# Kernel tuning notes

Measured on AMD Instinct MI355X. Metric: run time of the kernel, lower is better.

## Reference

```python
import jax, jax.numpy as jnp
import numpy as np

SR = 44100        # sample rate (init arg)
WIN = 442         # FFT window length from tensor[i:i+442]
HOP = 4           # loop stride
NBINS = 221       # kept spectrum bins x[:221]
THR = 0.01        # threshold passed to inner fftLayer
REL = 0.0594      # relative pitch-change threshold
BIN_HZ = 100.0    # argmax*100 -> frequency


def _windows_and_mag(tensor):
    n = tensor.shape[0]
    n_win = (n - WIN + HOP - 1) // HOP
    starts = jnp.arange(n_win) * HOP
    windows = tensor[starts[:, None] + jnp.arange(WIN)[None, :]]
    spec = jnp.fft.fft(windows, axis=-1)[:, :NBINS]           # complex64 [n_win, 221]
    spec = jnp.where(jnp.abs(spec) < THR, jnp.zeros_like(spec), spec)  # fftLayer threshold
    mag = jnp.abs(spec.real) + jnp.abs(spec.imag)             # |re| + |im|, as in forward
    return mag, starts


def setup_inputs() -> dict:
    key = jax.random.key(0)
    return {"tensor": jax.random.normal(key, (1_000_000,), dtype=jnp.float32)}


def reference(tensor):
    mag, starts = _windows_and_mag(tensor)
    # per-window dominant frequency: argmax bin * 100 Hz
    tmp = jnp.argmax(mag, axis=-1).astype(jnp.float32) * BIN_HZ    # [n_win]
    i_samp = starts.astype(jnp.float32)                            # sample index of each window

    def step(carry, x):
        maxF, Ftime = carry
        t, i = x
        cond = jnp.abs(maxF - t) > maxF * REL
        emit_f = maxF
        emit_d = (i - Ftime) * 1000.0 / SR
        maxF = jnp.where(cond, t, maxF)
        Ftime = jnp.where(cond, i, Ftime)
        return (maxF, Ftime), (cond, emit_f, emit_d)

    (maxF, Ftime), (flags, freqs, durs) = jax.lax.scan(
        step, (jnp.float32(0.0), jnp.float32(0.0)), (tmp, i_samp))
    # trailing append after the loop: (maxF, (i_last - Ftime)*1000/44100)
    final = jnp.stack([maxF, (i_samp[-1] - Ftime) * 1000.0 / SR])
    # flags marks windows where a note boundary was emitted; (freqs, durs) at those
    # positions are the (maxF, duration_ms) pairs the original appends to `out`.
    return flags, freqs, durs, final
```

## Files before the change

### kernel.cpp

```cpp
#include <hip/hip_runtime.h>

#define WIN 442
#define HOP 4
#define NBINS 221
#define LC 128
#define SPAN 960
#define B2 1024
#define NG 32

static __device__ __forceinline__ unsigned long long shflx64(unsigned long long v, int off) {
    unsigned int lo = (unsigned int)v, hi = (unsigned int)(v >> 32);
    lo = __shfl_xor(lo, off, 64);
    hi = __shfl_xor(hi, off, 64);
    return ((unsigned long long)hi << 32) | lo;
}

__global__ void k_tables(float2* __restrict__ g_tab, double2* __restrict__ TBR) {
    int t = blockIdx.x * blockDim.x + threadIdx.x;
    const double TWO_PI = 6.283185307179586476925287;
    if (t < WIN) {
        double ang = TWO_PI * (double)t / (double)WIN;
        g_tab[t] = make_float2((float)cos(ang), (float)(-sin(ang)));
    }
    if (t < NBINS) {
        int t4 = (4 * t) % WIN;
        double a4 = TWO_PI * (double)t4 / (double)WIN;
        TBR[t] = make_double2(cos(a4), sin(a4));
    }
}

__global__ __launch_bounds__(128) void k_slide(
    const float* __restrict__ x, int n, int n_win, int n_chunks,
    const float2* __restrict__ g_tab, const double2* __restrict__ TBRg,
    int* __restrict__ a_arr) {
    __shared__ float2 tab[WIN];
    __shared__ __align__(16) float Xs[SPAN];
    __shared__ __align__(16) float Ds_[LC * 4];
    __shared__ unsigned long long cand[LC][9];

    const int tid = threadIdx.x;
    const int lane = tid & 63;
    const int wc = tid >> 6;
    const int chunk = blockIdx.x;
    const int s0 = chunk * (LC * HOP);

    for (int t = tid; t < WIN; t += 128) tab[t] = g_tab[t];
    for (int i = tid; i < SPAN; i += 128) {
        int g = s0 + i;
        Xs[i] = (g < n) ? x[g] : 0.0f;
    }
    __syncthreads();
    for (int r = tid; r < LC * 4; r += 128) Ds_[r] = Xs[r + WIN] - Xs[r];
    __syncthreads();

    const int wlen = min(LC, n_win - chunk * LC);

    const int k0 = lane + 128 * wc, k1 = k0 + 64;
    const bool a0 = (k0 < NBINS), a1 = (k1 < NBINS);
    const int kk0 = a0 ? k0 : 0, kk1 = a1 ? k1 : 0;
    const unsigned int lo0 = 255u - (unsigned)k0, lo1 = 255u - (unsigned)k1;
    const float2 e1_0 = tab[kk0], e1_1 = tab[kk1];
    const float2 e2_0 = tab[2 * kk0], e2_1 = tab[2 * kk1];
    int t3 = 3 * kk0; if (t3 >= WIN) t3 -= WIN; const float2 e3_0 = tab[t3];
    t3 = 3 * kk1; if (t3 >= WIN) t3 -= WIN; const float2 e3_1 = tab[t3];
    double2 Rk0 = TBRg[kk0], Rk1 = TBRg[kk1];
    if (!a0) { Rk0.x = 0.0; Rk0.y = 0.0; }
    if (!a1) { Rk1.x = 0.0; Rk1.y = 0.0; }

    double S0r, S0i, S1r, S1i;
    {
        float xa = Xs[440], xb = Xs[441];
        S0r = (double)fmaf(xb, e1_0.x, xa);
        S0i = (double)(xb * e1_0.y);
        S1r = (double)fmaf(xb, e1_1.x, xa);
        S1i = (double)(xb * e1_1.y);
        const float4* Xq = (const float4*)Xs;
#pragma unroll 2
        for (int t = 109; t >= 0; --t) {
            float4 xv = Xq[t];
            float Dr0 = fmaf(xv.w, e3_0.x, fmaf(xv.z, e2_0.x, fmaf(xv.y, e1_0.x, xv.x)));
            float Di0 = fmaf(xv.w, e3_0.y, fmaf(xv.z, e2_0.y, xv.y * e1_0.y));
            double nr = fma(S0i, Rk0.y, fma(S0r, Rk0.x, (double)Dr0));
            double ni = fma(-S0r, Rk0.y, fma(S0i, Rk0.x, (double)Di0));
            S0r = nr; S0i = ni;
            float Dr1 = fmaf(xv.w, e3_1.x, fmaf(xv.z, e2_1.x, fmaf(xv.y, e1_1.x, xv.x)));
            float Di1 = fmaf(xv.w, e3_1.y, fmaf(xv.z, e2_1.y, xv.y * e1_1.y));
            nr = fma(S1i, Rk1.y, fma(S1r, Rk1.x, (double)Dr1));
            ni = fma(-S1r, Rk1.y, fma(S1i, Rk1.x, (double)Di1));
            S1r = nr; S1i = ni;
        }
    }
    if (!a0) { S0r = 0.0; S0i = 0.0; }
    if (!a1) { S1r = 0.0; S1i = 0.0; }

    const float4* Dq = (const float4*)Ds_;
    for (int b = 0; b < 16; ++b) {
        unsigned long long key[8];
#pragma unroll
        for (int u = 0; u < 8; ++u) {
            if (b | u) {
                float4 d = Dq[b * 8 + u - 1];
                float Dr0 = fmaf(d.w, e3_0.x, fmaf(d.z, e2_0.x, fmaf(d.y, e1_0.x, d.x)));
                float Di0 = fmaf(d.w, e3_0.y, fmaf(d.z, e2_0.y, d.y * e1_0.y));
                double nr = S0r + (double)Dr0;
                double ni = S0i + (double)Di0;
                S0r = fma(nr, Rk0.x, -(ni * Rk0.y));
                S0i = fma(nr, Rk0.y, ni * Rk0.x);
                float Dr1 = fmaf(d.w, e3_1.x, fmaf(d.z, e2_1.x, fmaf(d.y, e1_1.x, d.x)));
                float Di1 = fmaf(d.w, e3_1.y, fmaf(d.z, e2_1.y, d.y * e1_1.y));
                nr = S1r + (double)Dr1;
                ni = S1i + (double)Di1;
                S1r = fma(nr, Rk1.x, -(ni * Rk1.y));
                S1i = fma(nr, Rk1.y, ni * Rk1.x);
            }
            float m0 = (float)(fabs(S0r) + fabs(S0i));
            float m1 = (float)(fabs(S1r) + fabs(S1i));
            unsigned long long key0 = ((unsigned long long)__float_as_uint(m0) << 32) | lo0;
            unsigned long long key1 = ((unsigned long long)__float_as_uint(m1) << 32) | lo1;
            key[u] = (key1 > key0) ? key1 : key0;
        }
#pragma unroll
        for (int s = 0; s < 4; ++s) {
            const int off = 32 >> s;
#pragma unroll
            for (int u = 0; u < 8; ++u) {
                unsigned long long o = shflx64(key[u], off);
                if (o > key[u]) key[u] = o;
            }
        }
        if (lane < 4) {
#pragma unroll
            for (int u = 0; u < 8; ++u) cand[b * 8 + u][wc * 4 + lane] = key[u];
        }
    }
    __syncthreads();
    if (tid < wlen) {
        unsigned long long best = cand[tid][0];
#pragma unroll
        for (int i = 1; i < 8; ++i) {
            unsigned long long c = cand[tid][i];
            if (c > best) best = c;
        }
        a_arr[chunk * LC + tid] = 255 - (int)(best & 255u);
    }
}

__global__ __launch_bounds__(256) void k_maps(const int* __restrict__ a_arr, int n_win,
                                              int L2, int* __restrict__ M0) {
    __shared__ float tf[256];
    __shared__ int ti[256];
    int j = blockIdx.x;
    int wbeg = j * L2;
    int cnt = n_win - wbeg; if (cnt > L2) cnt = L2; if (cnt < 0) cnt = 0;
    for (int i = threadIdx.x; i < cnt; i += 256) {
        int a = a_arr[wbeg + i];
        ti[i] = a; tf[i] = 100.0f * (float)a;
    }
    __syncthreads();
    int b = threadIdx.x;
    if (b < NBINS) {
        float mF = 100.0f * (float)b;
        int bin = b, rw = -1;
        for (int i = 0; i < cnt; ++i) {
            float t = tf[i];
            if (fabsf(mF - t) > mF * 0.0594f) { mF = t; bin = ti[i]; rw = wbeg + i; }
        }
        M0[j * NBINS + b] = ((rw + 1) << 8) | bin;
    }
}

__global__ __launch_bounds__(256) void k_sm1(const int* __restrict__ M0,
                                             int* __restrict__ M1) {
    __shared__ int sm[32 * NBINS];
    int g = blockIdx.x;
    for (int i = threadIdx.x; i < 32 * NBINS; i += 256) sm[i] = M0[g * 32 * NBINS + i];
    __syncthreads();
    int b = threadIdx.x;
    if (b < NBINS) {
        int bin = b, rw = -1;
        for (int i = 0; i < 32; ++i) {
            int mp = sm[i * NBINS + bin];
            if (mp >> 8) { rw = (mp >> 8) - 1; bin = mp & 255; }
        }
        M1[g * NBINS + b] = ((rw + 1) << 8) | bin;
    }
}

__global__ __launch_bounds__(256) void k_emit(const int* __restrict__ a_arr,
    const int* __restrict__ M0, const int* __restrict__ M1, int n_win, int L2,
    float* __restrict__ flags, float* __restrict__ freqs, float* __restrict__ durs,
    float* __restrict__ out_final) {
    __shared__ int sm1[NG * NBINS];
    __shared__ float tf[256];
    __shared__ int e0s;
    int j = blockIdx.x;
    int g = j >> 5;
    int wbeg = j * L2;
    int cnt = n_win - wbeg; if (cnt > L2) cnt = L2;
    if (cnt <= 0) return;
    for (int i = threadIdx.x; i < NG * NBINS; i += 256) sm1[i] = M1[i];
    for (int i = threadIdx.x; i < cnt; i += 256) tf[i] = 100.0f * (float)a_arr[wbeg + i];
    __syncthreads();
    if (threadIdx.x == 0) {
        int bin = 0, rw = -1;
        for (int i = 0; i < g; ++i) {
            int mp = sm1[i * NBINS + bin];
            if (mp >> 8) { rw = (mp >> 8) - 1; bin = mp & 255; }
        }
        for (int i = g * 32; i < j; ++i) {
            int mp = M0[i * NBINS + bin];
            if (mp >> 8) { rw = (mp >> 8) - 1; bin = mp & 255; }
        }
        e0s = ((rw + 1) << 8) | bin;
    }
    __syncthreads();
    int t = threadIdx.x;
    if (t < cnt) {
        int st = e0s;
        float maxF = 100.0f * (float)(st & 255);
        int rw = (st >> 8) - 1;
        float Ftime = (rw < 0) ? 0.0f : 4.0f * (float)rw;
        for (int i = 0; i < t; ++i) {
            float tv = tf[i];
            if (fabsf(maxF - tv) > maxF * 0.0594f) {
                maxF = tv; Ftime = 4.0f * (float)(wbeg + i);
            }
        }
        int w = wbeg + t;
        float tv = tf[t];
        float iw = 4.0f * (float)w;
        bool cond = fabsf(maxF - tv) > maxF * 0.0594f;
        flags[w] = cond ? 1.0f : 0.0f;
        freqs[w] = maxF;
        durs[w] = (iw - Ftime) * 1000.0f / 44100.0f;
        if (w == n_win - 1) {
            float fMax = cond ? tv : maxF;
            float fT   = cond ? iw : Ftime;
            out_final[0] = fMax;
            out_final[1] = (iw - fT) * 1000.0f / 44100.0f;
        }
    }
}

extern "C" void kernel_launch(void* const* d_in, const int* in_sizes, int n_in,
                              void* d_out, int out_size, void* d_ws, size_t ws_size,
                              hipStream_t stream) {
    const float* x = (const float*)d_in[0];
    int n = in_sizes[0];
    int n_win = (n - WIN + HOP - 1) / HOP;
    float* out = (float*)d_out;
    char* ws = (char*)d_ws;

    int n_chunks = (n_win + LC - 1) / LC;
    int L2 = (n_win + B2 - 1) / B2;

    float2*  g_tab = (float2*)(ws + 0);
    double2* TBR   = (double2*)(ws + 4096);
    int* a_arr     = (int*)(ws + 8192);
    int* M0        = (int*)(ws + 1008640);
    int* M1        = (int*)(ws + 1914112);

    k_tables<<<dim3(2), dim3(256), 0, stream>>>(g_tab, TBR);
    k_slide<<<dim3(n_chunks), dim3(128), 0, stream>>>(x, n, n_win, n_chunks,
                                                      g_tab, TBR, a_arr);
    k_maps<<<dim3(B2), dim3(256), 0, stream>>>(a_arr, n_win, L2, M0);
    k_sm1<<<dim3(NG), dim3(256), 0, stream>>>(M0, M1);
    k_emit<<<dim3(B2), dim3(256), 0, stream>>>(a_arr, M0, M1, n_win, L2,
                                               out, out + (size_t)n_win,
                                               out + 2 * (size_t)n_win,
                                               out + 3 * (size_t)n_win);
}
```

Measured before the change: 178.3 us.

## Precompute twiddle tables at compile time, radix-8 initial DFT, stage M0 in LDS

Twiddle tables are now built at compile time with a constexpr Taylor-series sincos and placed in constant memory. This removes the k_tables launch and the per-block LDS table copy. The initial full-window DFT now processes 8 samples per step with a rotation by 8k, which halves the number of serial double-precision recurrence steps. k_emit also stages its group's M0 slice in shared memory so the serial prefix walk reads LDS instead of global memory. In exchange, shared memory use in k_emit grows, and the constexpr trig and the longer float accumulation chains may shift rounding slightly.

```diff
diff --git a/kernel.cpp b/kernel.cpp
--- a/kernel.cpp
+++ b/kernel.cpp
@@ -8,6 +8,53 @@
 #define B2 1024
 #define NG 32
 
+constexpr double kPI = 3.14159265358979323846264338327950288;
+
+constexpr double tsin_poly(double r) {
+    double t = r, s = r;
+    for (int n = 1; n <= 9; ++n) { t *= -(r * r) / ((2.0 * n) * (2.0 * n + 1.0)); s += t; }
+    return s;
+}
+constexpr double tcos_poly(double r) {
+    double t = 1.0, c = 1.0;
+    for (int n = 1; n <= 9; ++n) { t *= -(r * r) / ((2.0 * n - 1.0) * (2.0 * n)); c += t; }
+    return c;
+}
+struct SC { double s, c; };
+constexpr SC tsincos(double a) {
+    int q = (int)(a / (kPI / 2) + 0.5);
+    double r = a - q * (kPI / 2);
+    double sr = tsin_poly(r), cr = tcos_poly(r);
+    switch (q & 3) {
+        case 0: return {sr, cr};
+        case 1: return {cr, -sr};
+        case 2: return {-sr, -cr};
+        default: return {-cr, sr};
+    }
+}
+struct TabF { float c[WIN]; float s[WIN]; };
+constexpr TabF make_tabf() {
+    TabF t{};
+    for (int i = 0; i < WIN; ++i) {
+        SC sc = tsincos(2.0 * kPI * (double)i / 442.0);
+        t.c[i] = (float)sc.c; t.s[i] = (float)(-sc.s);
+    }
+    return t;
+}
+struct TabR { double c4[NBINS], s4[NBINS], c8[NBINS], s8[NBINS]; };
+constexpr TabR make_tabr() {
+    TabR t{};
+    for (int k = 0; k < NBINS; ++k) {
+        SC a = tsincos(2.0 * kPI * (double)((4 * k) % WIN) / 442.0);
+        t.c4[k] = a.c; t.s4[k] = a.s;
+        SC b = tsincos(2.0 * kPI * (double)((8 * k) % WIN) / 442.0);
+        t.c8[k] = b.c; t.s8[k] = b.s;
+    }
+    return t;
+}
+__constant__ TabF cTabF = make_tabf();
+__constant__ TabR cTabR = make_tabr();
+
 static __device__ __forceinline__ unsigned long long shflx64(unsigned long long v, int off) {
     unsigned int lo = (unsigned int)v, hi = (unsigned int)(v >> 32);
     lo = __shfl_xor(lo, off, 64);
@@ -15,25 +62,9 @@
     return ((unsigned long long)hi << 32) | lo;
 }
 
-__global__ void k_tables(float2* __restrict__ g_tab, double2* __restrict__ TBR) {
-    int t = blockIdx.x * blockDim.x + threadIdx.x;
-    const double TWO_PI = 6.283185307179586476925287;
-    if (t < WIN) {
-        double ang = TWO_PI * (double)t / (double)WIN;
-        g_tab[t] = make_float2((float)cos(ang), (float)(-sin(ang)));
-    }
-    if (t < NBINS) {
-        int t4 = (4 * t) % WIN;
-        double a4 = TWO_PI * (double)t4 / (double)WIN;
-        TBR[t] = make_double2(cos(a4), sin(a4));
-    }
-}
-
 __global__ __launch_bounds__(128) void k_slide(
     const float* __restrict__ x, int n, int n_win, int n_chunks,
-    const float2* __restrict__ g_tab, const double2* __restrict__ TBRg,
     int* __restrict__ a_arr) {
-    __shared__ float2 tab[WIN];
     __shared__ __align__(16) float Xs[SPAN];
     __shared__ __align__(16) float Ds_[LC * 4];
     __shared__ unsigned long long cand[LC][9];
@@ -44,7 +75,6 @@
     const int chunk = blockIdx.x;
     const int s0 = chunk * (LC * HOP);
 
-    for (int t = tid; t < WIN; t += 128) tab[t] = g_tab[t];
     for (int i = tid; i < SPAN; i += 128) {
         int g = s0 + i;
         Xs[i] = (g < n) ? x[g] : 0.0f;
@@ -59,34 +89,57 @@
     const bool a0 = (k0 < NBINS), a1 = (k1 < NBINS);
     const int kk0 = a0 ? k0 : 0, kk1 = a1 ? k1 : 0;
     const unsigned int lo0 = 255u - (unsigned)k0, lo1 = 255u - (unsigned)k1;
-    const float2 e1_0 = tab[kk0], e1_1 = tab[kk1];
-    const float2 e2_0 = tab[2 * kk0], e2_1 = tab[2 * kk1];
-    int t3 = 3 * kk0; if (t3 >= WIN) t3 -= WIN; const float2 e3_0 = tab[t3];
-    t3 = 3 * kk1; if (t3 >= WIN) t3 -= WIN; const float2 e3_1 = tab[t3];
-    double2 Rk0 = TBRg[kk0], Rk1 = TBRg[kk1];
-    if (!a0) { Rk0.x = 0.0; Rk0.y = 0.0; }
-    if (!a1) { Rk1.x = 0.0; Rk1.y = 0.0; }
+
+    float ec0[8], es0[8], ec1[8], es1[8];
+    {
+        int t0 = 0, t1 = 0;
+#pragma unroll
+        for (int m = 1; m < 8; ++m) {
+            t0 += kk0; if (t0 >= WIN) t0 -= WIN;
+            ec0[m] = cTabF.c[t0]; es0[m] = cTabF.s[t0];
+            t1 += kk1; if (t1 >= WIN) t1 -= WIN;
+            ec1[m] = cTabF.c[t1]; es1[m] = cTabF.s[t1];
+        }
+    }
+    double C40 = a0 ? cTabR.c4[kk0] : 0.0, S40 = a0 ? cTabR.s4[kk0] : 0.0;
+    double C41 = a1 ? cTabR.c4[kk1] : 0.0, S41 = a1 ? cTabR.s4[kk1] : 0.0;
+    const double C80 = cTabR.c8[kk0], S80 = cTabR.s8[kk0];
+    const double C81 = cTabR.c8[kk1], S81 = cTabR.s8[kk1];
 
     double S0r, S0i, S1r, S1i;
     {
         float xa = Xs[440], xb = Xs[441];
-        S0r = (double)fmaf(xb, e1_0.x, xa);
-        S0i = (double)(xb * e1_0.y);
-        S1r = (double)fmaf(xb, e1_1.x, xa);
-        S1i = (double)(xb * e1_1.y);
+        S0r = (double)fmaf(xb, ec0[1], xa);
+        S0i = (double)(xb * es0[1]);
+        S1r = (double)fmaf(xb, ec1[1], xa);
+        S1i = (double)(xb * es1[1]);
         const float4* Xq = (const float4*)Xs;
-#pragma unroll 2
-        for (int t = 109; t >= 0; --t) {
-            float4 xv = Xq[t];
-            float Dr0 = fmaf(xv.w, e3_0.x, fmaf(xv.z, e2_0.x, fmaf(xv.y, e1_0.x, xv.x)));
-            float Di0 = fmaf(xv.w, e3_0.y, fmaf(xv.z, e2_0.y, xv.y * e1_0.y));
-            double nr = fma(S0i, Rk0.y, fma(S0r, Rk0.x, (double)Dr0));
-            double ni = fma(-S0r, Rk0.y, fma(S0i, Rk0.x, (double)Di0));
+#pragma unroll 1
+        for (int t = 54; t >= 0; --t) {
+            float4 va = Xq[2 * t], vb = Xq[2 * t + 1];
+            float Dr0 = va.x;
+            Dr0 = fmaf(va.y, ec0[1], Dr0); Dr0 = fmaf(va.z, ec0[2], Dr0);
+            Dr0 = fmaf(va.w, ec0[3], Dr0); Dr0 = fmaf(vb.x, ec0[4], Dr0);
+            Dr0 = fmaf(vb.y, ec0[5], Dr0); Dr0 = fmaf(vb.z, ec0[6], Dr0);
+            Dr0 = fmaf(vb.w, ec0[7], Dr0);
+            float Di0 = va.y * es0[1];
+            Di0 = fmaf(va.z, es0[2], Di0); Di0 = fmaf(va.w, es0[3], Di0);
+            Di0 = fmaf(vb.x, es0[4], Di0); Di0 = fmaf(vb.y, es0[5], Di0);
+            Di0 = fmaf(vb.z, es0[6], Di0); Di0 = fmaf(vb.w, es0[7], Di0);
+            double nr = fma(S0r, C80, fma(S0i, S80, (double)Dr0));
+            double ni = fma(S0i, C80, fma(S0r, -S80, (double)Di0));
             S0r = nr; S0i = ni;
-            float Dr1 = fmaf(xv.w, e3_1.x, fmaf(xv.z, e2_1.x, fmaf(xv.y, e1_1.x, xv.x)));
-            float Di1 = fmaf(xv.w, e3_1.y, fmaf(xv.z, e2_1.y, xv.y * e1_1.y));
-            nr = fma(S1i, Rk1.y, fma(S1r, Rk1.x, (double)Dr1));
-            ni = fma(-S1r, Rk1.y, fma(S1i, Rk1.x, (double)Di1));
+            float Dr1 = va.x;
+            Dr1 = fmaf(va.y, ec1[1], Dr1); Dr1 = fmaf(va.z, ec1[2], Dr1);
+            Dr1 = fmaf(va.w, ec1[3], Dr1); Dr1 = fmaf(vb.x, ec1[4], Dr1);
+            Dr1 = fmaf(vb.y, ec1[5], Dr1); Dr1 = fmaf(vb.z, ec1[6], Dr1);
+            Dr1 = fmaf(vb.w, ec1[7], Dr1);
+            float Di1 = va.y * es1[1];
+            Di1 = fmaf(va.z, es1[2], Di1); Di1 = fmaf(va.w, es1[3], Di1);
+            Di1 = fmaf(vb.x, es1[4], Di1); Di1 = fmaf(vb.y, es1[5], Di1);
+            Di1 = fmaf(vb.z, es1[6], Di1); Di1 = fmaf(vb.w, es1[7], Di1);
+            nr = fma(S1r, C81, fma(S1i, S81, (double)Dr1));
+            ni = fma(S1i, C81, fma(S1r, -S81, (double)Di1));
             S1r = nr; S1i = ni;
         }
     }
@@ -100,18 +153,18 @@
         for (int u = 0; u < 8; ++u) {
             if (b | u) {
                 float4 d = Dq[b * 8 + u - 1];
-                float Dr0 = fmaf(d.w, e3_0.x, fmaf(d.z, e2_0.x, fmaf(d.y, e1_0.x, d.x)));
-                float Di0 = fmaf(d.w, e3_0.y, fmaf(d.z, e2_0.y, d.y * e1_0.y));
+                float Dr0 = fmaf(d.w, ec0[3], fmaf(d.z, ec0[2], fmaf(d.y, ec0[1], d.x)));
+                float Di0 = fmaf(d.w, es0[3], fmaf(d.z, es0[2], d.y * es0[1]));
                 double nr = S0r + (double)Dr0;
                 double ni = S0i + (double)Di0;
-                S0r = fma(nr, Rk0.x, -(ni * Rk0.y));
-                S0i = fma(nr, Rk0.y, ni * Rk0.x);
-                float Dr1 = fmaf(d.w, e3_1.x, fmaf(d.z, e2_1.x, fmaf(d.y, e1_1.x, d.x)));
-                float Di1 = fmaf(d.w, e3_1.y, fmaf(d.z, e2_1.y, d.y * e1_1.y));
+                S0r = fma(nr, C40, -(ni * S40));
+                S0i = fma(nr, S40, ni * C40);
+                float Dr1 = fmaf(d.w, ec1[3], fmaf(d.z, ec1[2], fmaf(d.y, ec1[1], d.x)));
+                float Di1 = fmaf(d.w, es1[3], fmaf(d.z, es1[2], d.y * es1[1]));
                 nr = S1r + (double)Dr1;
                 ni = S1i + (double)Di1;
-                S1r = fma(nr, Rk1.x, -(ni * Rk1.y));
-                S1i = fma(nr, Rk1.y, ni * Rk1.x);
+                S1r = fma(nr, C41, -(ni * S41));
+                S1i = fma(nr, S41, ni * C41);
             }
             float m0 = (float)(fabs(S0r) + fabs(S0i));
             float m1 = (float)(fabs(S1r) + fabs(S1i));
@@ -191,6 +244,7 @@
     float* __restrict__ flags, float* __restrict__ freqs, float* __restrict__ durs,
     float* __restrict__ out_final) {
     __shared__ int sm1[NG * NBINS];
+    __shared__ int sm0[32 * NBINS];
     __shared__ float tf[256];
     __shared__ int e0s;
     int j = blockIdx.x;
@@ -199,6 +253,7 @@
     int cnt = n_win - wbeg; if (cnt > L2) cnt = L2;
     if (cnt <= 0) return;
     for (int i = threadIdx.x; i < NG * NBINS; i += 256) sm1[i] = M1[i];
+    for (int i = threadIdx.x; i < 32 * NBINS; i += 256) sm0[i] = M0[g * 32 * NBINS + i];
     for (int i = threadIdx.x; i < cnt; i += 256) tf[i] = 100.0f * (float)a_arr[wbeg + i];
     __syncthreads();
     if (threadIdx.x == 0) {
@@ -207,8 +262,9 @@
             int mp = sm1[i * NBINS + bin];
             if (mp >> 8) { rw = (mp >> 8) - 1; bin = mp & 255; }
         }
-        for (int i = g * 32; i < j; ++i) {
-            int mp = M0[i * NBINS + bin];
+        int lim = j & 31;
+        for (int i = 0; i < lim; ++i) {
+            int mp = sm0[i * NBINS + bin];
             if (mp >> 8) { rw = (mp >> 8) - 1; bin = mp & 255; }
         }
         e0s = ((rw + 1) << 8) | bin;
@@ -254,15 +310,11 @@
     int n_chunks = (n_win + LC - 1) / LC;
     int L2 = (n_win + B2 - 1) / B2;
 
-    float2*  g_tab = (float2*)(ws + 0);
-    double2* TBR   = (double2*)(ws + 4096);
-    int* a_arr     = (int*)(ws + 8192);
-    int* M0        = (int*)(ws + 1008640);
-    int* M1        = (int*)(ws + 1914112);
-
-    k_tables<<<dim3(2), dim3(256), 0, stream>>>(g_tab, TBR);
-    k_slide<<<dim3(n_chunks), dim3(128), 0, stream>>>(x, n, n_win, n_chunks,
-                                                      g_tab, TBR, a_arr);
+    int* a_arr = (int*)(ws + 0);
+    int* M0    = (int*)(ws + 1000448);
+    int* M1    = (int*)(ws + 1905664);
+
+    k_slide<<<dim3(n_chunks), dim3(128), 0, stream>>>(x, n, n_win, n_chunks, a_arr);
     k_maps<<<dim3(B2), dim3(256), 0, stream>>>(a_arr, n_win, L2, M0);
     k_sm1<<<dim3(NG), dim3(256), 0, stream>>>(M0, M1);
     k_emit<<<dim3(B2), dim3(256), 0, stream>>>(a_arr, M0, M1, n_win, L2,
```

Result: no change. 180.0 us (+0.9%).
